# Performance work log

Hardware: AMD Instinct MI355X
Metric: run time of the kernel (lower is better)

Reference implementation:

```python
import jax, jax.numpy as jnp
import numpy as np

B, L, DL, DM, K = 8192, 1, 1024, 1024, 8


def setup_inputs() -> dict:
    key = jax.random.key(0)
    ks = jax.random.split(key, 8)
    s = lambda k, shape, sc=1.0: jax.random.normal(k, shape, jnp.float32) * sc
    return {
        "l_hidden": s(ks[0], (B, L, DL)),
        "m_hidden": s(ks[1], (B, L, DM)),
        "G_l_m": s(ks[2], (DL, K, DM)),   # randn'd each fwd in torch; exposed as input
        "G_m_l": s(ks[3], (DM, K, DL)),
        "l_fc1_w": s(ks[4], (256, DL), 0.02),
        "l_fc1_b": jnp.zeros((256,), jnp.float32),
        "l_fc2_w": s(ks[5], (DL, 256), 0.02),
        "l_fc2_b": jnp.zeros((DL,), jnp.float32),
        "m_fc1_w": s(ks[6], (128, DM), 0.02),
        "m_fc1_b": jnp.zeros((128,), jnp.float32),
        "m_fc2_w": s(ks[7], (DM, 128), 0.02),
        "m_fc2_b": jnp.zeros((DM,), jnp.float32),
    }


def _cross(h_a, h_b, G, g_vec):
    """One direction of the cross-share unit.
    h_a: [B,L,Da], h_b: [B,L,Db], G: [Da,K,Db], g_vec: [B,L,Da]. L must be 1.
    Broadcasts G over batch instead of torch's .repeat (same math, no 256GB copy).
    """
    b, l, da = h_a.shape
    k = G.shape[1]
    # l_hidden @ reshape(G, [Da, K*Db]) -> reshape to [B, L*K, Db]
    s = jnp.einsum('bld,dke->blke', h_a, G).reshape(b, l * k, -1)      # [B,L*K,Db]
    # tanh( shared @ h_b^T ) -> [B, L*K, L]
    t = jnp.tanh(jnp.einsum('bke,bse->bks', s, h_b))                    # [B,L*K,L]
    # reshape [B,L,K,L] -> permute [B,L,L,K] -> [B,L*L,K]
    t = t.reshape(b, l, k, l).transpose(0, 1, 3, 2).reshape(b, l * l, k)
    g = jnp.tile(g_vec, (1, k, 1))                                      # [B,L*K,Da] (L=1 -> [B,K,Da])
    vec = jnp.matmul(t, g)                                              # [B,L*L,Da]
    attn = jax.nn.softmax(vec, axis=-1)
    out = h_a + attn * h_a
    return out, attn


def reference(l_hidden, m_hidden, G_l_m, G_m_l,
              l_fc1_w, l_fc1_b, l_fc2_w, l_fc2_b,
              m_fc1_w, m_fc1_b, m_fc2_w, m_fc2_b):
    # dropout(0.3) is identity in eval mode
    G_vec_l = (l_hidden @ l_fc1_w.T + l_fc1_b) @ l_fc2_w.T + l_fc2_b   # [B,L,DL]
    G_vec_m = (m_hidden @ m_fc1_w.T + m_fc1_b) @ m_fc2_w.T + m_fc2_b   # [B,L,DM]
    l_out, l_attn = _cross(l_hidden, m_hidden, G_l_m, G_vec_l)
    m_out, m_attn = _cross(m_hidden, l_hidden, G_m_l, G_vec_m)
    return l_out, m_out, l_attn, m_attn
```

## Files before the change

kernel.cpp:

```cpp
#include <hip/hip_runtime.h>


#define NB 8192
#define DD 1024

typedef __bf16 bf16x8 __attribute__((ext_vector_type(8)));
typedef float f32x4 __attribute__((ext_vector_type(4)));

__device__ __forceinline__ unsigned short f2bf(float f) {
  unsigned u = __float_as_uint(f);
  u += 0x7FFFu + ((u >> 16) & 1u);
  return (unsigned short)(u >> 16);
}
__device__ __forceinline__ float bf2f(unsigned short h) {
  return __uint_as_float(((unsigned)h) << 16);
}

__device__ __forceinline__ size_t bidx(int n, int k) {
  return ((size_t)(n >> 4) << 14) + ((k >> 5) << 9) + (((k >> 3) & 3) << 7) +
         ((n & 15) << 3) + (k & 7);
}

__global__ __launch_bounds__(256) void split_cast_k(
    const float* __restrict__ in, unsigned short* __restrict__ hi,
    unsigned short* __restrict__ lo, int n4) {
  int i = blockIdx.x * 256 + threadIdx.x;
  if (i >= n4) return;
  float4 v = reinterpret_cast<const float4*>(in)[i];
  float vv[4] = {v.x, v.y, v.z, v.w};
  unsigned short hh[4], ll[4];
#pragma unroll
  for (int c = 0; c < 4; ++c) {
    hh[c] = f2bf(vv[c]);
    ll[c] = f2bf(vv[c] - bf2f(hh[c]));
  }
  reinterpret_cast<ushort4*>(hi)[i] = make_ushort4(hh[0], hh[1], hh[2], hh[3]);
  reinterpret_cast<ushort4*>(lo)[i] = make_ushort4(ll[0], ll[1], ll[2], ll[3]);
}

__global__ __launch_bounds__(256) void transpose_split_k(
    const float* __restrict__ G, unsigned short* __restrict__ bhi,
    unsigned short* __restrict__ blo) {
  __shared__ float t[32][33];
  int c0 = blockIdx.x * 32;
  int d0 = blockIdx.y * 32;
  int tx = threadIdx.x & 31;
  int tg = threadIdx.x >> 5;
#pragma unroll
  for (int s = 0; s < 4; ++s) {
    int dr = tg * 4 + s;
    t[dr][tx] = G[(size_t)(d0 + dr) * 8192 + c0 + tx];
  }
  __syncthreads();
#pragma unroll
  for (int s = 0; s < 4; ++s) {
    int cr = tg * 4 + s;
    float v = t[tx][cr];
    size_t o = bidx(c0 + cr, d0 + tx);
    unsigned short h = f2bf(v);
    bhi[o] = h;
    blo[o] = f2bf(v - bf2f(h));
  }
}

__global__ __launch_bounds__(256) void wct_k(
    const float* __restrict__ w1, const float* __restrict__ b1,
    const float* __restrict__ w2, const float* __restrict__ b2, int J,
    unsigned short* __restrict__ bhi, unsigned short* __restrict__ blo,
    float* __restrict__ bc) {
  __shared__ float w2row[256];
  int n = blockIdx.x;
  int tid = threadIdx.x;
  if (tid < J) w2row[tid] = w2[n * J + tid];
  __syncthreads();
#pragma unroll
  for (int s = 0; s < 4; ++s) {
    int i = tid + s * 256;
    float acc = 0.f;
    for (int j = 0; j < J; ++j) acc = fmaf(w2row[j], w1[j * 1024 + i], acc);
    size_t o = bidx(8192 + n, i);
    unsigned short h = f2bf(acc);
    bhi[o] = h;
    blo[o] = f2bf(acc - bf2f(h));
  }
  if (tid == 0) {
    float acc = 0.f;
    for (int j = 0; j < J; ++j) acc = fmaf(w2row[j], b1[j], acc);
    bc[n] = acc + b2[n];
  }
}

#define SBAR() do { asm volatile("" ::: "memory"); __builtin_amdgcn_s_barrier(); asm volatile("" ::: "memory"); } while (0)
#define WAITV0() asm volatile("s_waitcnt vmcnt(0)" ::: "memory")
#define WAITV4() asm volatile("s_waitcnt vmcnt(4)" ::: "memory")

#define GLOAD(SRC, DST)                                              \
  __builtin_amdgcn_global_load_lds(                                  \
      (const __attribute__((address_space(1))) void*)(SRC),          \
      (__attribute__((address_space(3))) void*)(lds + (DST)), 16, 0, 0)

__global__ __launch_bounds__(512, 1) void gemm_k(
    const unsigned short* __restrict__ Ahi_, const unsigned short* __restrict__ Alo_,
    const unsigned short* __restrict__ Bhi_, const unsigned short* __restrict__ Blo_,
    const float* __restrict__ hb, float* __restrict__ gvec, float* __restrict__ x) {
  __shared__ __align__(16) char lds[65536];
  const char* Ah = (const char*)Ahi_;
  const char* Al = (const char*)Alo_;
  const char* Bh = (const char*)Bhi_;
  const char* Bl = (const char*)Blo_;

  const int tid = threadIdx.x;
  const int lane = tid & 63;
  const int wid = tid >> 6;
  const int wm = wid >> 2, wn = wid & 3;

  const int bid = blockIdx.x;
  const int xcd = bid & 7;
  const int j = bid >> 3;
  const int by = xcd * 4 + (j & 3);
  const int bx = j >> 2;
  const int m0 = by * 256;
  const int n0 = bx * 256;
  const bool isg = (n0 >= 8192);
  const int nt = isg ? 16 : 48;

  const int rowl = tid >> 3;
  const int colsw = ((tid & 7) ^ ((tid >> 3) & 7)) << 4;
  const int s0 = ((lane >> 4) ^ (lane & 7)) << 4;
  const int s1 = s0 ^ 64;

  f32x4 acc[4][4][2] = {};

  auto stage = [&](int tl, int par, int q) {
    const char* mat = ((tl >> 4) == 1) ? Al : Ah;
    const char* src = mat + (size_t)(m0 + q * 128 + rowl) * 2048 + ((tl & 15) << 7) + colsw;
    const int dst = par * 32768 + q * 16384 + wid * 1024;
    GLOAD(src, dst);
    GLOAD(src + 64 * 2048, dst + 8192);
  };

  auto ldA = [&](bf16x8 (*d)[2], int qa, int cb) {
    const char* p = lds + cb + qa * 16384 + (wm * 64 + (lane & 15)) * 128;
#pragma unroll
    for (int f = 0; f < 4; ++f) {
      d[f][0] = *reinterpret_cast<const bf16x8*>(p + f * 2048 + s0);
      d[f][1] = *reinterpret_cast<const bf16x8*>(p + f * 2048 + s1);
    }
  };
  auto ldBdir = [&](bf16x8 (*d)[2], int qn, int tl) {
    const char* base = ((tl >> 4) == 2) ? Bl : Bh;
#pragma unroll
    for (int g = 0; g < 2; ++g) {
      const size_t chunk =
          ((size_t)(n0 >> 4) + qn * 8 + wn * 2 + g) * 32 + ((tl & 15) << 1);
      const char* p = base + chunk * 1024 + lane * 16;
      d[g][0] = *reinterpret_cast<const bf16x8*>(p);
      d[g][1] = *reinterpret_cast<const bf16x8*>(p + 1024);
    }
  };
  auto mm = [&](f32x4 (*ac)[2], bf16x8 (*aa)[2], bf16x8 (*bb)[2]) {
#pragma unroll
    for (int f = 0; f < 4; ++f)
#pragma unroll
      for (int g = 0; g < 2; ++g) {
        ac[f][g] = __builtin_amdgcn_mfma_f32_16x16x32_bf16(aa[f][0], bb[g][0], ac[f][g], 0, 0, 0);
        ac[f][g] = __builtin_amdgcn_mfma_f32_16x16x32_bf16(aa[f][1], bb[g][1], ac[f][g], 0, 0, 0);
      }
  };

  bf16x8 af[4][2], af2[4][2], bv[2][2], bv2[2][2];

  stage(0, 0, 0); stage(0, 0, 1);
  ldBdir(bv, 0, 0);
  __builtin_amdgcn_sched_barrier(0);
  WAITV4();
  SBAR();
  ldA(af, 0, 0);

  for (int t = 0; t < nt; ++t) {
    const int cb = (t & 1) * 32768;
    const int cbN = cb ^ 32768;
    const int parN = (t + 1) & 1;
    const int tn = (t + 1 < nt) ? (t + 1) : (nt - 1);
    ldBdir(bv2, 1, t);
    stage(tn, parN, 0);
    __builtin_amdgcn_s_setprio(1);
    mm(acc[0], af, bv);
    __builtin_amdgcn_s_setprio(0);
    ldA(af2, 1, cb);
    __builtin_amdgcn_s_setprio(1);
    mm(acc[1], af, bv2);
    __builtin_amdgcn_s_setprio(0);
    WAITV0();
    SBAR();
    ldA(af, 0, cbN);
    stage(tn, parN, 1);
    __builtin_amdgcn_s_setprio(1);
    mm(acc[2], af2, bv2);
    __builtin_amdgcn_s_setprio(0);
    __builtin_amdgcn_s_setprio(1);
    mm(acc[3], af2, bv);
    __builtin_amdgcn_s_setprio(0);
    __builtin_amdgcn_sched_barrier(0);
    ldBdir(bv, 0, tn);
    __builtin_amdgcn_sched_barrier(0);
    WAITV4();
    SBAR();
  }

  const int coll = lane & 15;
  const int rg = (lane >> 4) * 4;
  if (isg) {
#pragma unroll
    for (int q = 0; q < 4; ++q) {
      const int qm = (q >= 2);
      const int qn = (q == 1 || q == 2);
#pragma unroll
      for (int f = 0; f < 4; ++f)
#pragma unroll
        for (int rr = 0; rr < 4; ++rr) {
          const int row = m0 + qm * 128 + wm * 64 + f * 16 + rg + rr;
#pragma unroll
          for (int g = 0; g < 2; ++g) {
            const int gcol = (n0 - 8192) + qn * 128 + wn * 32 + g * 16 + coll;
            gvec[(size_t)row * 1024 + gcol] = acc[q][f][g][rr];
          }
        }
    }
  } else {
    const int kidx = n0 >> 10;
    const int ebase = (n0 & 1023) + wn * 32 + coll;
#pragma unroll
    for (int qm = 0; qm < 2; ++qm) {
      f32x4 (*acA)[2] = acc[qm ? 3 : 0];
      f32x4 (*acB)[2] = acc[qm ? 2 : 1];
#pragma unroll
      for (int f = 0; f < 4; ++f)
#pragma unroll
        for (int rr = 0; rr < 4; ++rr) {
          const int row = m0 + qm * 128 + wm * 64 + f * 16 + rg + rr;
          const float* hr = hb + (size_t)row * 1024 + ebase;
          float tmp = acA[f][0][rr] * hr[0] + acA[f][1][rr] * hr[16] +
                      acB[f][0][rr] * hr[128] + acB[f][1][rr] * hr[144];
#pragma unroll
          for (int s = 1; s < 16; s <<= 1) tmp += __shfl_xor(tmp, s);
          if (coll == 0) atomicAdd(&x[row * 8 + kidx], tmp);
        }
    }
  }
}

__global__ __launch_bounds__(256) void finalize_k(
    const float* __restrict__ xk, const float* __restrict__ gvec,
    const float* __restrict__ bc, const float* __restrict__ ha,
    float* __restrict__ out, float* __restrict__ attn) {
  int b = blockIdx.x;
  int tid = threadIdx.x;
  float S = 0.f;
#pragma unroll
  for (int k = 0; k < 8; ++k) S += tanhf(xk[b * 8 + k]);
  float v[4];
  float mx = -3.4e38f;
#pragma unroll
  for (int s = 0; s < 4; ++s) {
    int d = tid + s * 256;
    v[s] = S * (gvec[(size_t)b * 1024 + d] + bc[d]);
    mx = fmaxf(mx, v[s]);
  }
  __shared__ float red[8];
#pragma unroll
  for (int off = 32; off >= 1; off >>= 1) mx = fmaxf(mx, __shfl_xor(mx, off));
  int lane = tid & 63, w = tid >> 6;
  if (lane == 0) red[w] = mx;
  __syncthreads();
  float m = fmaxf(fmaxf(red[0], red[1]), fmaxf(red[2], red[3]));
  float e[4], sum = 0.f;
#pragma unroll
  for (int s = 0; s < 4; ++s) { e[s] = __expf(v[s] - m); sum += e[s]; }
#pragma unroll
  for (int off = 32; off >= 1; off >>= 1) sum += __shfl_xor(sum, off);
  if (lane == 0) red[4 + w] = sum;
  __syncthreads();
  float inv = 1.f / (red[4] + red[5] + red[6] + red[7]);
#pragma unroll
  for (int s = 0; s < 4; ++s) {
    int d = tid + s * 256;
    float a = e[s] * inv;
    attn[(size_t)b * 1024 + d] = a;
    float h = ha[(size_t)b * 1024 + d];
    out[(size_t)b * 1024 + d] = fmaf(a, h, h);
  }
}

extern "C" void kernel_launch(void* const* d_in, const int* in_sizes, int n_in,
                              void* d_out, int out_size, void* d_ws, size_t ws_size,
                              hipStream_t stream) {
  const float* l_hidden = (const float*)d_in[0];
  const float* m_hidden = (const float*)d_in[1];
  const float* G_l_m = (const float*)d_in[2];
  const float* G_m_l = (const float*)d_in[3];
  const float* l_fc1_w = (const float*)d_in[4];
  const float* l_fc1_b = (const float*)d_in[5];
  const float* l_fc2_w = (const float*)d_in[6];
  const float* l_fc2_b = (const float*)d_in[7];
  const float* m_fc1_w = (const float*)d_in[8];
  const float* m_fc1_b = (const float*)d_in[9];
  const float* m_fc2_w = (const float*)d_in[10];
  const float* m_fc2_b = (const float*)d_in[11];
  float* out = (float*)d_out;

  char* ws = (char*)d_ws;
  unsigned short* Ahi = (unsigned short*)(ws);
  unsigned short* Alo = (unsigned short*)(ws + 16777216);
  unsigned short* Bhi = (unsigned short*)(ws + 33554432);
  unsigned short* Blo = (unsigned short*)(ws + 52428800);
  float* gvec = (float*)(ws + 71303168);
  float* x = (float*)(ws + 104857600);
  float* bc = (float*)(ws + 105381888);

  hipMemsetAsync(x, 0, 2 * NB * 8 * sizeof(float), stream);

  const size_t BD = (size_t)NB * DD;
  dim3 gemmGrid(1152);

  split_cast_k<<<(int)(BD / 4 / 256), 256, 0, stream>>>(l_hidden, Ahi, Alo, (int)(BD / 4));
  transpose_split_k<<<dim3(256, 32), 256, 0, stream>>>(G_l_m, Bhi, Blo);
  wct_k<<<1024, 256, 0, stream>>>(l_fc1_w, l_fc1_b, l_fc2_w, l_fc2_b, 256, Bhi, Blo, bc);
  gemm_k<<<gemmGrid, 512, 0, stream>>>(Ahi, Alo, Bhi, Blo, m_hidden, gvec, x);
  finalize_k<<<NB, 256, 0, stream>>>(x, gvec, bc, l_hidden, out, out + 2 * BD);

  split_cast_k<<<(int)(BD / 4 / 256), 256, 0, stream>>>(m_hidden, Ahi, Alo, (int)(BD / 4));
  transpose_split_k<<<dim3(256, 32), 256, 0, stream>>>(G_m_l, Bhi, Blo);
  wct_k<<<1024, 256, 0, stream>>>(m_fc1_w, m_fc1_b, m_fc2_w, m_fc2_b, 128, Bhi, Blo, bc);
  gemm_k<<<gemmGrid, 512, 0, stream>>>(Ahi, Alo, Bhi, Blo, l_hidden, gvec, x + NB * 8);
  finalize_k<<<NB, 256, 0, stream>>>(x + NB * 8, gvec, bc, m_hidden, out + BD, out + 3 * BD);
}
```

Measured before the change: 1.173 ms.

## Merge prep kernels, double-buffer B fragments in GEMM loop, vectorize finalize

Three preprocessing kernels (split-cast of activations, transpose-split of G, fused weight product) are merged into one launch that dispatches on block index. In the GEMM main loop, B fragments are now double-buffered across two register sets with the loop unrolled by two, so next-tile B loads are issued earlier and the full vmcnt(0) wait is relaxed to vmcnt(4). The finalize kernel switches to float4 loads and stores with a contiguous per-thread element mapping. Register pressure in the GEMM rises with the extra B buffers, and the unroll by two assumes an even tile count.

```diff
diff --git a/kernel.cpp b/kernel.cpp
--- a/kernel.cpp
+++ b/kernel.cpp
@@ -21,78 +21,75 @@
          ((n & 15) << 3) + (k & 7);
 }
 
-__global__ __launch_bounds__(256) void split_cast_k(
-    const float* __restrict__ in, unsigned short* __restrict__ hi,
-    unsigned short* __restrict__ lo, int n4) {
-  int i = blockIdx.x * 256 + threadIdx.x;
-  if (i >= n4) return;
-  float4 v = reinterpret_cast<const float4*>(in)[i];
-  float vv[4] = {v.x, v.y, v.z, v.w};
-  unsigned short hh[4], ll[4];
-#pragma unroll
-  for (int c = 0; c < 4; ++c) {
-    hh[c] = f2bf(vv[c]);
-    ll[c] = f2bf(vv[c] - bf2f(hh[c]));
-  }
-  reinterpret_cast<ushort4*>(hi)[i] = make_ushort4(hh[0], hh[1], hh[2], hh[3]);
-  reinterpret_cast<ushort4*>(lo)[i] = make_ushort4(ll[0], ll[1], ll[2], ll[3]);
-}
-
-__global__ __launch_bounds__(256) void transpose_split_k(
-    const float* __restrict__ G, unsigned short* __restrict__ bhi,
-    unsigned short* __restrict__ blo) {
-  __shared__ float t[32][33];
-  int c0 = blockIdx.x * 32;
-  int d0 = blockIdx.y * 32;
-  int tx = threadIdx.x & 31;
-  int tg = threadIdx.x >> 5;
-#pragma unroll
-  for (int s = 0; s < 4; ++s) {
-    int dr = tg * 4 + s;
-    t[dr][tx] = G[(size_t)(d0 + dr) * 8192 + c0 + tx];
-  }
-  __syncthreads();
-#pragma unroll
-  for (int s = 0; s < 4; ++s) {
-    int cr = tg * 4 + s;
-    float v = t[tx][cr];
-    size_t o = bidx(c0 + cr, d0 + tx);
-    unsigned short h = f2bf(v);
-    bhi[o] = h;
-    blo[o] = f2bf(v - bf2f(h));
-  }
-}
-
-__global__ __launch_bounds__(256) void wct_k(
+__global__ __launch_bounds__(256) void prep_k(
+    const float* __restrict__ h, const float* __restrict__ G,
     const float* __restrict__ w1, const float* __restrict__ b1,
     const float* __restrict__ w2, const float* __restrict__ b2, int J,
-    unsigned short* __restrict__ bhi, unsigned short* __restrict__ blo,
+    unsigned short* __restrict__ Ahi, unsigned short* __restrict__ Alo,
+    unsigned short* __restrict__ Bhi, unsigned short* __restrict__ Blo,
     float* __restrict__ bc) {
+  __shared__ float t[32][33];
   __shared__ float w2row[256];
-  int n = blockIdx.x;
-  int tid = threadIdx.x;
-  if (tid < J) w2row[tid] = w2[n * J + tid];
-  __syncthreads();
-#pragma unroll
-  for (int s = 0; s < 4; ++s) {
-    int i = tid + s * 256;
-    float acc = 0.f;
-    for (int j = 0; j < J; ++j) acc = fmaf(w2row[j], w1[j * 1024 + i], acc);
-    size_t o = bidx(8192 + n, i);
-    unsigned short h = f2bf(acc);
-    bhi[o] = h;
-    blo[o] = f2bf(acc - bf2f(h));
+  const int bid = blockIdx.x;
+  const int tid = threadIdx.x;
+  if (bid < 8192) {
+    int i = bid * 256 + tid;
+    float4 v = reinterpret_cast<const float4*>(h)[i];
+    float vv[4] = {v.x, v.y, v.z, v.w};
+    unsigned short hh[4], ll[4];
+#pragma unroll
+    for (int c = 0; c < 4; ++c) {
+      hh[c] = f2bf(vv[c]);
+      ll[c] = f2bf(vv[c] - bf2f(hh[c]));
+    }
+    reinterpret_cast<ushort4*>(Ahi)[i] = make_ushort4(hh[0], hh[1], hh[2], hh[3]);
+    reinterpret_cast<ushort4*>(Alo)[i] = make_ushort4(ll[0], ll[1], ll[2], ll[3]);
+  } else if (bid < 16384) {
+    const int b = bid - 8192;
+    const int c0 = (b & 255) * 32;
+    const int d0 = (b >> 8) * 32;
+    const int tx = tid & 31;
+    const int tg = tid >> 5;
+#pragma unroll
+    for (int s = 0; s < 4; ++s) {
+      int dr = tg * 4 + s;
+      t[dr][tx] = G[(size_t)(d0 + dr) * 8192 + c0 + tx];
+    }
+    __syncthreads();
+#pragma unroll
+    for (int s = 0; s < 4; ++s) {
+      int cr = tg * 4 + s;
+      float v = t[tx][cr];
+      size_t o = bidx(c0 + cr, d0 + tx);
+      unsigned short hh = f2bf(v);
+      Bhi[o] = hh;
+      Blo[o] = f2bf(v - bf2f(hh));
+    }
+  } else {
+    const int n = bid - 16384;
+    if (tid < J) w2row[tid] = w2[n * J + tid];
+    __syncthreads();
+#pragma unroll
+    for (int s = 0; s < 4; ++s) {
+      int i = tid + s * 256;
+      float acc = 0.f;
+      for (int j = 0; j < J; ++j) acc = fmaf(w2row[j], w1[j * 1024 + i], acc);
+      size_t o = bidx(8192 + n, i);
+      unsigned short hh = f2bf(acc);
+      Bhi[o] = hh;
+      Blo[o] = f2bf(acc - bf2f(hh));
+    }
+    if (tid == 0) {
+      float acc = 0.f;
+      for (int j = 0; j < J; ++j) acc = fmaf(w2row[j], b1[j], acc);
+      bc[n] = acc + b2[n];
+    }
   }
-  if (tid == 0) {
-    float acc = 0.f;
-    for (int j = 0; j < J; ++j) acc = fmaf(w2row[j], b1[j], acc);
-    bc[n] = acc + b2[n];
-  }
 }
 
 #define SBAR() do { asm volatile("" ::: "memory"); __builtin_amdgcn_s_barrier(); asm volatile("" ::: "memory"); } while (0)
-#define WAITV0() asm volatile("s_waitcnt vmcnt(0)" ::: "memory")
 #define WAITV4() asm volatile("s_waitcnt vmcnt(4)" ::: "memory")
+#define WAITV8() asm volatile("s_waitcnt vmcnt(8)" ::: "memory")
 
 #define GLOAD(SRC, DST)                                              \
   __builtin_amdgcn_global_load_lds(                                  \
@@ -168,44 +165,49 @@
       }
   };
 
-  bf16x8 af[4][2], af2[4][2], bv[2][2], bv2[2][2];
+  bf16x8 af[4][2], af2[4][2];
+  bf16x8 b0A[2][2], b1A[2][2], b0B[2][2], b1B[2][2];
 
   stage(0, 0, 0); stage(0, 0, 1);
-  ldBdir(bv, 0, 0);
-  __builtin_amdgcn_sched_barrier(0);
-  WAITV4();
+  ldBdir(b0A, 0, 0);
+  ldBdir(b1A, 1, 0);
+  WAITV8();
   SBAR();
   ldA(af, 0, 0);
 
-  for (int t = 0; t < nt; ++t) {
+  auto body = [&](int t, bf16x8 (*b0c)[2], bf16x8 (*b1c)[2],
+                  bf16x8 (*b0n)[2], bf16x8 (*b1n)[2]) {
     const int cb = (t & 1) * 32768;
     const int cbN = cb ^ 32768;
     const int parN = (t + 1) & 1;
     const int tn = (t + 1 < nt) ? (t + 1) : (nt - 1);
-    ldBdir(bv2, 1, t);
     stage(tn, parN, 0);
     __builtin_amdgcn_s_setprio(1);
-    mm(acc[0], af, bv);
+    mm(acc[0], af, b0c);
     __builtin_amdgcn_s_setprio(0);
     ldA(af2, 1, cb);
+    ldBdir(b0n, 0, tn);
     __builtin_amdgcn_s_setprio(1);
-    mm(acc[1], af, bv2);
+    mm(acc[1], af, b1c);
     __builtin_amdgcn_s_setprio(0);
-    WAITV0();
+    WAITV4();
     SBAR();
     ldA(af, 0, cbN);
     stage(tn, parN, 1);
     __builtin_amdgcn_s_setprio(1);
-    mm(acc[2], af2, bv2);
+    mm(acc[2], af2, b1c);
     __builtin_amdgcn_s_setprio(0);
+    ldBdir(b1n, 1, tn);
     __builtin_amdgcn_s_setprio(1);
-    mm(acc[3], af2, bv);
+    mm(acc[3], af2, b0c);
     __builtin_amdgcn_s_setprio(0);
-    __builtin_amdgcn_sched_barrier(0);
-    ldBdir(bv, 0, tn);
-    __builtin_amdgcn_sched_barrier(0);
     WAITV4();
     SBAR();
+  };
+
+  for (int tt = 0; tt < nt; tt += 2) {
+    body(tt, b0A, b1A, b0B, b1B);
+    body(tt + 1, b0B, b1B, b0A, b1A);
   }
 
   const int coll = lane & 15;
@@ -259,14 +261,11 @@
   float S = 0.f;
 #pragma unroll
   for (int k = 0; k < 8; ++k) S += tanhf(xk[b * 8 + k]);
-  float v[4];
-  float mx = -3.4e38f;
-#pragma unroll
-  for (int s = 0; s < 4; ++s) {
-    int d = tid + s * 256;
-    v[s] = S * (gvec[(size_t)b * 1024 + d] + bc[d]);
-    mx = fmaxf(mx, v[s]);
-  }
+  float4 g4 = reinterpret_cast<const float4*>(gvec)[b * 256 + tid];
+  float4 c4 = reinterpret_cast<const float4*>(bc)[tid];
+  float v[4] = {S * (g4.x + c4.x), S * (g4.y + c4.y),
+                S * (g4.z + c4.z), S * (g4.w + c4.w)};
+  float mx = fmaxf(fmaxf(v[0], v[1]), fmaxf(v[2], v[3]));
   __shared__ float red[8];
 #pragma unroll
   for (int off = 32; off >= 1; off >>= 1) mx = fmaxf(mx, __shfl_xor(mx, off));
@@ -282,14 +281,13 @@
   if (lane == 0) red[4 + w] = sum;
   __syncthreads();
   float inv = 1.f / (red[4] + red[5] + red[6] + red[7]);
-#pragma unroll
-  for (int s = 0; s < 4; ++s) {
-    int d = tid + s * 256;
-    float a = e[s] * inv;
-    attn[(size_t)b * 1024 + d] = a;
-    float h = ha[(size_t)b * 1024 + d];
-    out[(size_t)b * 1024 + d] = fmaf(a, h, h);
-  }
+  float4 h4 = reinterpret_cast<const float4*>(ha)[b * 256 + tid];
+  float4 a4, o4;
+  a4.x = e[0] * inv; a4.y = e[1] * inv; a4.z = e[2] * inv; a4.w = e[3] * inv;
+  o4.x = fmaf(a4.x, h4.x, h4.x); o4.y = fmaf(a4.y, h4.y, h4.y);
+  o4.z = fmaf(a4.z, h4.z, h4.z); o4.w = fmaf(a4.w, h4.w, h4.w);
+  reinterpret_cast<float4*>(attn)[b * 256 + tid] = a4;
+  reinterpret_cast<float4*>(out)[b * 256 + tid] = o4;
 }
 
 extern "C" void kernel_launch(void* const* d_in, const int* in_sizes, int n_in,
@@ -320,18 +318,17 @@
 
   hipMemsetAsync(x, 0, 2 * NB * 8 * sizeof(float), stream);
 
-  const size_t BD = (size_t)NB * DD;
   dim3 gemmGrid(1152);
-
-  split_cast_k<<<(int)(BD / 4 / 256), 256, 0, stream>>>(l_hidden, Ahi, Alo, (int)(BD / 4));
-  transpose_split_k<<<dim3(256, 32), 256, 0, stream>>>(G_l_m, Bhi, Blo);
-  wct_k<<<1024, 256, 0, stream>>>(l_fc1_w, l_fc1_b, l_fc2_w, l_fc2_b, 256, Bhi, Blo, bc);
+  dim3 prepGrid(17408);
+
+  prep_k<<<prepGrid, 256, 0, stream>>>(l_hidden, G_l_m, l_fc1_w, l_fc1_b,
+                                       l_fc2_w, l_fc2_b, 256, Ahi, Alo, Bhi, Blo, bc);
   gemm_k<<<gemmGrid, 512, 0, stream>>>(Ahi, Alo, Bhi, Blo, m_hidden, gvec, x);
-  finalize_k<<<NB, 256, 0, stream>>>(x, gvec, bc, l_hidden, out, out + 2 * BD);
-
-  split_cast_k<<<(int)(BD / 4 / 256), 256, 0, stream>>>(m_hidden, Ahi, Alo, (int)(BD / 4));
-  transpose_split_k<<<dim3(256, 32), 256, 0, stream>>>(G_m_l, Bhi, Blo);
-  wct_k<<<1024, 256, 0, stream>>>(m_fc1_w, m_fc1_b, m_fc2_w, m_fc2_b, 128, Bhi, Blo, bc);
+  finalize_k<<<NB, 256, 0, stream>>>(x, gvec, bc, l_hidden, out, out + 2 * (size_t)NB * DD);
+
+  prep_k<<<prepGrid, 256, 0, stream>>>(m_hidden, G_m_l, m_fc1_w, m_fc1_b,
+                                       m_fc2_w, m_fc2_b, 128, Ahi, Alo, Bhi, Blo, bc);
   gemm_k<<<gemmGrid, 512, 0, stream>>>(Ahi, Alo, Bhi, Blo, l_hidden, gvec, x + NB * 8);
-  finalize_k<<<NB, 256, 0, stream>>>(x + NB * 8, gvec, bc, m_hidden, out + BD, out + 3 * BD);
-}
+  finalize_k<<<NB, 256, 0, stream>>>(x + NB * 8, gvec, bc, m_hidden,
+                                     out + (size_t)NB * DD, out + 3 * (size_t)NB * DD);
+}
```

New measurement: 1.476 ms. 1.26x slower.
